# Kernel optimization log

Measured on AMD Instinct MI355X. Metric: run time of the kernel, lower is better.

The kernel has to match this reference:

```python
import jax, jax.numpy as jnp
import numpy as np
from jax import lax

B, S, H, T = 64, 512, 1024, 24


def setup_inputs() -> dict:
    key = jax.random.key(0)
    k1, k2, k3, k4, k5 = jax.random.split(key, 5)
    feats = jax.random.normal(k1, (B, S, H), dtype=jnp.float32)
    target = jax.random.randint(k2, (B, S), 0, T)  # tag ids (argmax of original one-hot target)
    # descending-sorted lengths -> prefix mask, matching the torch code's sorted-batch assumption
    lengths = jnp.sort(jax.random.randint(k3, (B,), S // 2, S + 1))[::-1]
    mask = jnp.arange(S)[None, :] < lengths[:, None]  # (B,S) bool
    # hidden2tag params (uniform init ~ nn.Linear default scale)
    bound = 1.0 / np.sqrt(H)
    W = jax.random.uniform(k4, (T, H), minval=-bound, maxval=bound, dtype=jnp.float32)
    b = jax.random.uniform(k5, (T,), minval=-bound, maxval=bound, dtype=jnp.float32)
    transition = jnp.zeros((T, T), dtype=jnp.float32)
    return {"feats": feats, "target": target, "mask": mask, "W": W, "b": b, "transition": transition}


def reference(feats, target, mask, W, b, transition):
    # emission scores: (B,S,T)
    emission = jnp.einsum("bsh,th->bst", feats, W) + b
    # gold path score
    sc = jnp.take_along_axis(emission, target[:, :, None], axis=2).squeeze(-1)  # (B,S)
    sc = sc.at[:, 1:].add(transition[target[:, :-1], target[:, 1:]])
    total_score = (sc * mask.astype(emission.dtype)).sum(axis=1)  # (B,)
    # forward algorithm (log-partition) as a scan over time
    p0 = emission[:, 0]  # (B,T)
    emis_t = jnp.swapaxes(emission[:, 1:], 0, 1)  # (S-1,B,T)
    mask_t = jnp.swapaxes(mask[:, 1:], 0, 1)      # (S-1,B)

    def step(p, xs):
        emit_i, m_i = xs
        # log_sum[b, prev, cur] = p[b, prev] + transition[prev, cur] + emit_i[b, cur]
        new_p = jax.nn.logsumexp(p[:, :, None] + transition[None, :, :] + emit_i[:, None, :], axis=1)
        return jnp.where(m_i[:, None], new_p, p), None

    p, _ = lax.scan(step, p0, (emis_t, mask_t))
    log_Z = jax.nn.logsumexp(p, axis=1)  # (B,)
    loss = -jnp.mean(total_score - log_Z)
    return loss, emission
```

## Files before the change

### kernel.cpp

```cpp
#include <hip/hip_runtime.h>
#include <cstdint>
#include <math.h>

#define B_ 64
#define S_ 512
#define H_ 1024
#define T_ 24

typedef unsigned int u32;
#define GLD_LDS16(g, l)                                                        \
    __builtin_amdgcn_global_load_lds(                                          \
        (const __attribute__((address_space(1))) u32*)(g),                     \
        (__attribute__((address_space(3))) u32*)(l), 16, 0, 0)

__device__ __forceinline__ float rl_f32(float x, int sl) {
    return __uint_as_float(__builtin_amdgcn_readlane(__float_as_uint(x), sl));
}

__global__ __launch_bounds__(512, 4) void gemm_kernel(const float* __restrict__ feats,
                                                      const float* __restrict__ W,
                                                      const float* __restrict__ bias,
                                                      float* __restrict__ emission) {
    __shared__ float4 tile4[2][1024];
    const int tid  = threadIdx.x;
    const int lane = tid & 63;
    const int w    = __builtin_amdgcn_readfirstlane(tid >> 6);
    const int t0   = w * 3;
    const long row0 = (long)blockIdx.x * 64;
    const float* fbase = feats + row0 * H_;

    float Wreg[3][16];
#pragma unroll
    for (int t = 0; t < 3; ++t) {
        const float* wr = W + (long)(t0 + t) * H_ + lane * 16;
#pragma unroll
        for (int m4 = 0; m4 < 4; ++m4) {
            const float4 v = *(const float4*)(wr + m4 * 4);
            Wreg[t][m4 * 4 + 0] = v.x;
            Wreg[t][m4 * 4 + 1] = v.y;
            Wreg[t][m4 * 4 + 2] = v.z;
            Wreg[t][m4 * 4 + 3] = v.w;
        }
    }

    const float* g0 = fbase + (long)lane * H_ + (2 * w) * 4;
    const float* g1 = g0 + 4;
#define STAGE(c, buf)                                                          \
    do {                                                                       \
        GLD_LDS16(g0 + (c) * 64, &tile4[(buf)][(2 * w) * 64]);                 \
        GLD_LDS16(g1 + (c) * 64, &tile4[(buf)][(2 * w + 1) * 64]);             \
    } while (0)

    float acc[3] = {0.f, 0.f, 0.f};
    STAGE(0, 0);

    for (int c = 0; c < 16; ++c) {
        __syncthreads();
        if (c + 1 < 16) STAGE(c + 1, (c + 1) & 1);
        const float4* tb = tile4[c & 1];
#pragma unroll
        for (int i = 0; i < 16; ++i) {
            const float4 fv = tb[i * 64 + lane];
            const int sl = 4 * c + (i >> 2);
            const int m = (i & 3) * 4;
#pragma unroll
            for (int t = 0; t < 3; ++t) {
                acc[t] = fmaf(fv.x, rl_f32(Wreg[t][m + 0], sl), acc[t]);
                acc[t] = fmaf(fv.y, rl_f32(Wreg[t][m + 1], sl), acc[t]);
                acc[t] = fmaf(fv.z, rl_f32(Wreg[t][m + 2], sl), acc[t]);
                acc[t] = fmaf(fv.w, rl_f32(Wreg[t][m + 3], sl), acc[t]);
            }
        }
    }

    float* out = emission + (row0 + lane) * T_ + t0;
#pragma unroll
    for (int t = 0; t < 3; ++t) out[t] = acc[t] + bias[t0 + t];
#undef STAGE
}

__global__ __launch_bounds__(64) void score_kernel(const float* __restrict__ emission,
                                                   const int* __restrict__ target,
                                                   const int* __restrict__ mask,
                                                   const float* __restrict__ trans,
                                                   float* __restrict__ ws_score) {
    const int b = blockIdx.x;
    const int lane = threadIdx.x;
    float sum = 0.f;
    for (int s = lane; s < S_; s += 64) {
        if (mask[b * S_ + s]) {
            const int tg = target[b * S_ + s];
            float v = emission[((long)b * S_ + s) * T_ + tg];
            if (s > 0) v += trans[target[b * S_ + s - 1] * T_ + tg];
            sum += v;
        }
    }
#pragma unroll
    for (int off = 32; off; off >>= 1) sum += __shfl_down(sum, off);
    if (lane == 0) ws_score[b] = sum;
}

#define DECL_E(i) const float E##i = __expf(trans[(i) * T_ + jj]);
#define FMA4(i0, i1, i2, i3)                                                   \
    s0 = fmaf(rl_f32(q, i0), E##i0, s0);                                       \
    s1 = fmaf(rl_f32(q, i1), E##i1, s1);                                       \
    s2 = fmaf(rl_f32(q, i2), E##i2, s2);                                       \
    s3 = fmaf(rl_f32(q, i3), E##i3, s3);

__global__ __launch_bounds__(64, 1) void scan_kernel(const float* __restrict__ emission,
                                                     const int* __restrict__ mask,
                                                     const float* __restrict__ trans,
                                                     float* __restrict__ ws_logZ) {
    const int b = blockIdx.x;
    const int j = threadIdx.x;
    const int jj = j < 24 ? j : 23;

    const float* em = emission + (long)b * S_ * T_;
    const int* mk = mask + b * S_;

    int mc = 0;
#pragma unroll
    for (int k = 0; k < 8; ++k) mc += mk[j + k * 64];
#pragma unroll
    for (int off = 32; off; off >>= 1) mc += __shfl_xor(mc, off);
    const int len = __builtin_amdgcn_readfirstlane(mc);

    DECL_E(0)  DECL_E(1)  DECL_E(2)  DECL_E(3)  DECL_E(4)  DECL_E(5)
    DECL_E(6)  DECL_E(7)  DECL_E(8)  DECL_E(9)  DECL_E(10) DECL_E(11)
    DECL_E(12) DECL_E(13) DECL_E(14) DECL_E(15) DECL_E(16) DECL_E(17)
    DECL_E(18) DECL_E(19) DECL_E(20) DECL_E(21) DECL_E(22) DECL_E(23)

    float q = (j < 24) ? __expf(em[j]) : 0.f;
    float C = 0.f;

    float lb[8];
#pragma unroll
    for (int k = 0; k < 8; ++k) lb[k] = em[(1 + k) * T_ + jj];

    for (int sb = 1; sb < S_; sb += 16) {
#pragma unroll
        for (int k = 0; k < 16; ++k) {
            const int s = sb + k;
            const float X = __expf(lb[k & 7]);
            const int sp = s + 8;
            lb[k & 7] = (sp < S_) ? em[sp * T_ + jj] : 0.f;

            if (s < len) {
                float s0 = 0.f, s1 = 0.f, s2 = 0.f, s3 = 0.f;
                FMA4(0, 1, 2, 3)
                FMA4(4, 5, 6, 7)
                FMA4(8, 9, 10, 11)
                FMA4(12, 13, 14, 15)
                FMA4(16, 17, 18, 19)
                FMA4(20, 21, 22, 23)
                q = ((s0 + s1) + (s2 + s3)) * X;
            }
        }
        const float r = rl_f32(q, 0);
        q *= (1.0f / r);
        C += __logf(r);
    }

    float ex = (j < 24) ? q : 0.f;
#pragma unroll
    for (int off = 32; off; off >>= 1) ex += __shfl_down(ex, off);
    if (j == 0) ws_logZ[b] = C + __logf(ex);
}

__global__ __launch_bounds__(64) void finalize_kernel(const float* __restrict__ ws_score,
                                                      const float* __restrict__ ws_logZ,
                                                      float* __restrict__ out) {
    const int l = threadIdx.x;
    float v = ws_score[l] - ws_logZ[l];
#pragma unroll
    for (int off = 32; off; off >>= 1) v += __shfl_down(v, off);
    if (l == 0) out[0] = -v * (1.0f / B_);
}

extern "C" void kernel_launch(void* const* d_in, const int* in_sizes, int n_in,
                              void* d_out, int out_size, void* d_ws, size_t ws_size,
                              hipStream_t stream) {
    const float* feats  = (const float*)d_in[0];
    const int*   target = (const int*)d_in[1];
    const int*   mask   = (const int*)d_in[2];
    const float* W      = (const float*)d_in[3];
    const float* bias   = (const float*)d_in[4];
    const float* trans  = (const float*)d_in[5];

    float* out = (float*)d_out;
    float* emission = out + 1;
    float* ws_score = (float*)d_ws;
    float* ws_logZ  = ws_score + 64;

    gemm_kernel<<<512, 512, 0, stream>>>(feats, W, bias, emission);
    score_kernel<<<64, 64, 0, stream>>>(emission, target, mask, trans, ws_score);
    scan_kernel<<<64, 64, 0, stream>>>(emission, mask, trans, ws_logZ);
    finalize_kernel<<<1, 64, 0, stream>>>(ws_score, ws_logZ, out);
}
```

Baseline: 306.1 us.

## Use split-bf16 MFMA GEMM and fuse score/finalize into scan kernel

The emission GEMM moves from a readlane-broadcast FP32 FMA loop to bf16 MFMA 16x16x32 instructions. Each operand is split into high and low bf16 halves, and three MFMAs per tile approximate FP32 accuracy. A small kernel pre-converts W into padded bf16 hi/lo arrays. The gold-score computation and the final reduction are folded into the scan kernel via an atomicAdd, which removes two launches. The bf16x3 split may give slightly lower accuracy than true FP32, and the atomic makes the summation order nondeterministic.

Result: faster. 285.0 us (-6.9%).

```diff
diff --git a/kernel.cpp b/kernel.cpp
--- a/kernel.cpp
+++ b/kernel.cpp
@@ -6,98 +6,103 @@
 #define S_ 512
 #define H_ 1024
 #define T_ 24
+#define TP_ 32
 
 typedef unsigned int u32;
-#define GLD_LDS16(g, l)                                                        \
-    __builtin_amdgcn_global_load_lds(                                          \
-        (const __attribute__((address_space(1))) u32*)(g),                     \
-        (__attribute__((address_space(3))) u32*)(l), 16, 0, 0)
+typedef unsigned short u16;
+typedef __attribute__((ext_vector_type(8))) short short8v;
+typedef __attribute__((ext_vector_type(4))) float f32x4;
+typedef __attribute__((ext_vector_type(4))) u32 uint4v;
 
 __device__ __forceinline__ float rl_f32(float x, int sl) {
     return __uint_as_float(__builtin_amdgcn_readlane(__float_as_uint(x), sl));
 }
 
-__global__ __launch_bounds__(512, 4) void gemm_kernel(const float* __restrict__ feats,
-                                                      const float* __restrict__ W,
-                                                      const float* __restrict__ bias,
-                                                      float* __restrict__ emission) {
-    __shared__ float4 tile4[2][1024];
+__device__ __forceinline__ void split_pk(float f0, float f1, u32& hpk, u32& lpk) {
+    const u32 u0 = __float_as_uint(f0), u1 = __float_as_uint(f1);
+    const u32 t1 = u1 & 0xffff0000u;
+    hpk = (u0 >> 16) | t1;
+    const float fl0 = f0 - __uint_as_float(u0 & 0xffff0000u);
+    const float fl1 = f1 - __uint_as_float(t1);
+    lpk = (__float_as_uint(fl0) >> 16) | (__float_as_uint(fl1) & 0xffff0000u);
+}
+
+__global__ __launch_bounds__(256) void wcvt_kernel(const float* __restrict__ W,
+                                                   u16* __restrict__ Wh,
+                                                   u16* __restrict__ Wl,
+                                                   float* __restrict__ out) {
+    const int i = blockIdx.x * 256 + threadIdx.x;
+    if (i == 0) out[0] = 0.f;
+    const int t = i >> 10;
+    const float f = (t < T_) ? W[i] : 0.f;
+    const u32 u = __float_as_uint(f);
+    const u32 rh = u + 0x7fffu + ((u >> 16) & 1u);
+    const u16 hb = (u16)(rh >> 16);
+    const float fh = __uint_as_float((u32)hb << 16);
+    const float fl = f - fh;
+    const u32 u2 = __float_as_uint(fl);
+    const u32 rl2 = u2 + 0x7fffu + ((u2 >> 16) & 1u);
+    Wh[i] = hb;
+    Wl[i] = (u16)(rl2 >> 16);
+}
+
+__global__ __launch_bounds__(256) void gemm_kernel(const float* __restrict__ feats,
+                                                   const u16* __restrict__ Wh,
+                                                   const u16* __restrict__ Wl,
+                                                   const float* __restrict__ bias,
+                                                   float* __restrict__ emission) {
     const int tid  = threadIdx.x;
     const int lane = tid & 63;
-    const int w    = __builtin_amdgcn_readfirstlane(tid >> 6);
-    const int t0   = w * 3;
-    const long row0 = (long)blockIdx.x * 64;
-    const float* fbase = feats + row0 * H_;
-
-    float Wreg[3][16];
-#pragma unroll
-    for (int t = 0; t < 3; ++t) {
-        const float* wr = W + (long)(t0 + t) * H_ + lane * 16;
-#pragma unroll
-        for (int m4 = 0; m4 < 4; ++m4) {
-            const float4 v = *(const float4*)(wr + m4 * 4);
-            Wreg[t][m4 * 4 + 0] = v.x;
-            Wreg[t][m4 * 4 + 1] = v.y;
-            Wreg[t][m4 * 4 + 2] = v.z;
-            Wreg[t][m4 * 4 + 3] = v.w;
-        }
-    }
-
-    const float* g0 = fbase + (long)lane * H_ + (2 * w) * 4;
-    const float* g1 = g0 + 4;
-#define STAGE(c, buf)                                                          \
-    do {                                                                       \
-        GLD_LDS16(g0 + (c) * 64, &tile4[(buf)][(2 * w) * 64]);                 \
-        GLD_LDS16(g1 + (c) * 64, &tile4[(buf)][(2 * w + 1) * 64]);             \
-    } while (0)
-
-    float acc[3] = {0.f, 0.f, 0.f};
-    STAGE(0, 0);
-
-    for (int c = 0; c < 16; ++c) {
-        __syncthreads();
-        if (c + 1 < 16) STAGE(c + 1, (c + 1) & 1);
-        const float4* tb = tile4[c & 1];
-#pragma unroll
-        for (int i = 0; i < 16; ++i) {
-            const float4 fv = tb[i * 64 + lane];
-            const int sl = 4 * c + (i >> 2);
-            const int m = (i & 3) * 4;
-#pragma unroll
-            for (int t = 0; t < 3; ++t) {
-                acc[t] = fmaf(fv.x, rl_f32(Wreg[t][m + 0], sl), acc[t]);
-                acc[t] = fmaf(fv.y, rl_f32(Wreg[t][m + 1], sl), acc[t]);
-                acc[t] = fmaf(fv.z, rl_f32(Wreg[t][m + 2], sl), acc[t]);
-                acc[t] = fmaf(fv.w, rl_f32(Wreg[t][m + 3], sl), acc[t]);
-            }
-        }
-    }
-
-    float* out = emission + (row0 + lane) * T_ + t0;
-#pragma unroll
-    for (int t = 0; t < 3; ++t) out[t] = acc[t] + bias[t0 + t];
-#undef STAGE
-}
-
-__global__ __launch_bounds__(64) void score_kernel(const float* __restrict__ emission,
-                                                   const int* __restrict__ target,
-                                                   const int* __restrict__ mask,
-                                                   const float* __restrict__ trans,
-                                                   float* __restrict__ ws_score) {
-    const int b = blockIdx.x;
-    const int lane = threadIdx.x;
-    float sum = 0.f;
-    for (int s = lane; s < S_; s += 64) {
-        if (mask[b * S_ + s]) {
-            const int tg = target[b * S_ + s];
-            float v = emission[((long)b * S_ + s) * T_ + tg];
-            if (s > 0) v += trans[target[b * S_ + s - 1] * T_ + tg];
-            sum += v;
-        }
-    }
-#pragma unroll
-    for (int off = 32; off; off >>= 1) sum += __shfl_down(sum, off);
-    if (lane == 0) ws_score[b] = sum;
+    const int wv   = tid >> 6;
+    const int r16  = lane & 15;
+    const int g    = lane >> 4;
+    const int mtile = blockIdx.x * 4 + wv;
+
+    const float* ap  = feats + ((long)mtile * 16 + r16) * H_ + g * 8;
+    const u16* bh0p = Wh + r16 * H_ + g * 8;
+    const u16* bl0p = Wl + r16 * H_ + g * 8;
+    const u16* bh1p = Wh + (r16 + 16) * H_ + g * 8;
+    const u16* bl1p = Wl + (r16 + 16) * H_ + g * 8;
+
+    f32x4 acc0 = {0.f, 0.f, 0.f, 0.f};
+    f32x4 acc1 = {0.f, 0.f, 0.f, 0.f};
+
+#pragma unroll 4
+    for (int kk = 0; kk < H_ / 32; ++kk) {
+        const int ko = kk * 32;
+        const float4 a0 = *(const float4*)(ap + ko);
+        const float4 a1 = *(const float4*)(ap + ko + 4);
+        const short8v bh0 = *(const short8v*)(bh0p + ko);
+        const short8v bl0 = *(const short8v*)(bl0p + ko);
+        const short8v bh1 = *(const short8v*)(bh1p + ko);
+        const short8v bl1 = *(const short8v*)(bl1p + ko);
+
+        u32 h0, l0, h1, l1, h2, l2, h3, l3;
+        split_pk(a0.x, a0.y, h0, l0);
+        split_pk(a0.z, a0.w, h1, l1);
+        split_pk(a1.x, a1.y, h2, l2);
+        split_pk(a1.z, a1.w, h3, l3);
+        const uint4v hv = {h0, h1, h2, h3};
+        const uint4v lv = {l0, l1, l2, l3};
+        const short8v ah = __builtin_bit_cast(short8v, hv);
+        const short8v al = __builtin_bit_cast(short8v, lv);
+
+        acc0 = __builtin_amdgcn_mfma_f32_16x16x32_bf16(al, bh0, acc0, 0, 0, 0);
+        acc0 = __builtin_amdgcn_mfma_f32_16x16x32_bf16(ah, bl0, acc0, 0, 0, 0);
+        acc0 = __builtin_amdgcn_mfma_f32_16x16x32_bf16(ah, bh0, acc0, 0, 0, 0);
+        acc1 = __builtin_amdgcn_mfma_f32_16x16x32_bf16(al, bh1, acc1, 0, 0, 0);
+        acc1 = __builtin_amdgcn_mfma_f32_16x16x32_bf16(ah, bl1, acc1, 0, 0, 0);
+        acc1 = __builtin_amdgcn_mfma_f32_16x16x32_bf16(ah, bh1, acc1, 0, 0, 0);
+    }
+
+    const float b0 = bias[r16];
+    const float b1 = (r16 + 16 < T_) ? bias[r16 + 16] : 0.f;
+    float* op = emission + ((long)mtile * 16 + g * 4) * T_;
+#pragma unroll
+    for (int r = 0; r < 4; ++r) {
+        op[r * T_ + r16] = acc0[r] + b0;
+        if (r16 + 16 < T_) op[r * T_ + r16 + 16] = acc1[r] + b1;
+    }
 }
 
 #define DECL_E(i) const float E##i = __expf(trans[(i) * T_ + jj]);
@@ -108,9 +113,10 @@
     s3 = fmaf(rl_f32(q, i3), E##i3, s3);
 
 __global__ __launch_bounds__(64, 1) void scan_kernel(const float* __restrict__ emission,
+                                                     const int* __restrict__ target,
                                                      const int* __restrict__ mask,
                                                      const float* __restrict__ trans,
-                                                     float* __restrict__ ws_logZ) {
+                                                     float* __restrict__ out) {
     const int b = blockIdx.x;
     const int j = threadIdx.x;
     const int jj = j < 24 ? j : 23;
@@ -164,17 +170,25 @@
     float ex = (j < 24) ? q : 0.f;
 #pragma unroll
     for (int off = 32; off; off >>= 1) ex += __shfl_down(ex, off);
-    if (j == 0) ws_logZ[b] = C + __logf(ex);
-}
-
-__global__ __launch_bounds__(64) void finalize_kernel(const float* __restrict__ ws_score,
-                                                      const float* __restrict__ ws_logZ,
-                                                      float* __restrict__ out) {
-    const int l = threadIdx.x;
-    float v = ws_score[l] - ws_logZ[l];
-#pragma unroll
-    for (int off = 32; off; off >>= 1) v += __shfl_down(v, off);
-    if (l == 0) out[0] = -v * (1.0f / B_);
+
+    float ssum = 0.f;
+#pragma unroll
+    for (int kk = 0; kk < S_ / 64; ++kk) {
+        const int s = j + kk * 64;
+        if (mk[s]) {
+            const int tg = target[b * S_ + s];
+            float v = em[s * T_ + tg];
+            if (s > 0) v += trans[target[b * S_ + s - 1] * T_ + tg];
+            ssum += v;
+        }
+    }
+#pragma unroll
+    for (int off = 32; off; off >>= 1) ssum += __shfl_down(ssum, off);
+
+    if (j == 0) {
+        const float logZ = C + __logf(ex);
+        atomicAdd(out, (logZ - ssum) * (1.0f / B_));
+    }
 }
 
 extern "C" void kernel_launch(void* const* d_in, const int* in_sizes, int n_in,
@@ -189,11 +203,10 @@
 
     float* out = (float*)d_out;
     float* emission = out + 1;
-    float* ws_score = (float*)d_ws;
-    float* ws_logZ  = ws_score + 64;
-
-    gemm_kernel<<<512, 512, 0, stream>>>(feats, W, bias, emission);
-    score_kernel<<<64, 64, 0, stream>>>(emission, target, mask, trans, ws_score);
-    scan_kernel<<<64, 64, 0, stream>>>(emission, mask, trans, ws_logZ);
-    finalize_kernel<<<1, 64, 0, stream>>>(ws_score, ws_logZ, out);
-}
+    u16* Wh = (u16*)d_ws;
+    u16* Wl = Wh + TP_ * H_;
+
+    wcvt_kernel<<<(TP_ * H_) / 256, 256, 0, stream>>>(W, Wh, Wl, out);
+    gemm_kernel<<<512, 256, 0, stream>>>(feats, Wh, Wl, bias, emission);
+    scan_kernel<<<64, 64, 0, stream>>>(emission, target, mask, trans, out);
+}
```
